# Kernel tuning notes

Hardware: AMD Instinct MI355X
Metric: run time of the kernel (lower is better)

## Reference

```python
import jax, jax.numpy as jnp
import numpy as np

N_EMBED = 8192
EMBED_DIM = 4
BETA = 0.25


def setup_inputs() -> dict:
    key = jax.random.key(0)
    k1, k2 = jax.random.split(key)
    z = jax.random.normal(k1, (8, EMBED_DIM, 64, 64), dtype=jnp.float32)
    # torch init: uniform(-1/n_embed, 1/n_embed)
    embed_w = jax.random.uniform(k2, (N_EMBED, EMBED_DIM), dtype=jnp.float32,
                                 minval=-1.0 / N_EMBED, maxval=1.0 / N_EMBED)
    return {"z": z, "embed_w": embed_w}


def reference(z, embed_w):
    # z: [B, C, H, W] -> [B, H, W, C]
    z_nhwc = jnp.transpose(z, (0, 2, 3, 1))
    z_flat = z_nhwc.reshape(-1, EMBED_DIM)  # [N, D]
    # squared L2 distances: ||z||^2 + ||e||^2 - 2 z e^T  -> [N, n_embed]
    d = (jnp.sum(z_flat * z_flat, axis=1, keepdims=True)
         + jnp.sum(embed_w * embed_w, axis=1)
         - 2.0 * z_flat @ embed_w.T)
    min_idx = jnp.argmin(d, axis=1)  # [N] int
    z_q = embed_w[min_idx].reshape(z_nhwc.shape)  # [B, H, W, C]
    sg = jax.lax.stop_gradient
    loss = (jnp.mean((sg(z_q) - z_nhwc) ** 2)
            + BETA * jnp.mean((z_q - sg(z_nhwc)) ** 2))
    # straight-through estimator
    z_q_ste = z_nhwc + sg(z_q - z_nhwc)
    z_q_out = jnp.transpose(z_q_ste, (0, 3, 1, 2))  # back to [B, C, H, W]
    return z_q_out, loss, min_idx
```

## Files before the change

### kernel.cpp

```cpp
#include <hip/hip_runtime.h>
#include <math.h>

typedef float v2f __attribute__((ext_vector_type(2)));

#define N_POINTS 32768
#define NUM_EMBED 8192
#define NPAIRS 4096
#define CH 64
#define CPC (NUM_EMBED / CH)
#define PAIRS (NPAIRS / CH)
#define PPT 8
#define RB 1024
#define RPB (RB / 64)
#define CSTRIDE 4096

__global__ void vq_prep_kernel(const float4* __restrict__ E, v2f* __restrict__ Epk) {
    int p = blockIdx.x * 256 + threadIdx.x;
    if (p < NPAIRS) {
        float4 a = E[2 * p];
        float4 b = E[2 * p + 1];
        Epk[4 * p + 0] = (v2f){a.x, b.x};
        Epk[4 * p + 1] = (v2f){a.y, b.y};
        Epk[4 * p + 2] = (v2f){a.z, b.z};
        Epk[4 * p + 3] = (v2f){a.w, b.w};
    }
}

__device__ __forceinline__ v2f pk_mul(v2f a, v2f b) {
    v2f d; asm("v_pk_mul_f32 %0, %1, %2" : "=v"(d) : "v"(a), "v"(b)); return d;
}
__device__ __forceinline__ v2f pk_fma(v2f a, v2f b, v2f c) {
    v2f d; asm("v_pk_fma_f32 %0, %1, %2, %3" : "=v"(d) : "v"(a), "v"(b), "v"(c)); return d;
}

__device__ __forceinline__ unsigned int fkey(float f) {
    unsigned int b = __float_as_uint(f);
    return b ^ (0x80000000u | (unsigned int)((int)b >> 31));
}

__global__ __launch_bounds__(256) void vq_filter_kernel(
        const float* __restrict__ z, const v2f* __restrict__ Epk,
        float* __restrict__ cmax) {
    __shared__ alignas(16) v2f sE[PAIRS * 4];

    const int c = blockIdx.y;
    if (threadIdx.x < PAIRS * 2) {
        ((float4*)sE)[threadIdx.x] =
            ((const float4*)(Epk + (size_t)c * PAIRS * 4))[threadIdx.x];
    }

    const int n0 = blockIdx.x * (256 * PPT) + threadIdx.x;

    v2f zv[PPT][4];
    #pragma unroll
    for (int p = 0; p < PPT; ++p) {
        int n = n0 + p * 256;
        int b = n >> 12, hw = n & 4095;
        const float* zp = z + b * 16384 + hw;
        zv[p][0] = (v2f){zp[0], zp[0]};
        zv[p][1] = (v2f){zp[CSTRIDE], zp[CSTRIDE]};
        zv[p][2] = (v2f){zp[2 * CSTRIDE], zp[2 * CSTRIDE]};
        zv[p][3] = (v2f){zp[3 * CSTRIDE], zp[3 * CSTRIDE]};
    }

    __syncthreads();

    float run[PPT];
    #pragma unroll
    for (int p = 0; p < PPT; ++p) run[p] = -__builtin_inff();

    const float4* sE4 = (const float4*)sE;
    #pragma unroll 2
    for (int t = 0; t < PAIRS; ++t) {
        float4 E01 = sE4[2 * t];
        float4 E23 = sE4[2 * t + 1];
        v2f e0 = {E01.x, E01.y};
        v2f e1 = {E01.z, E01.w};
        v2f e2 = {E23.x, E23.y};
        v2f e3 = {E23.z, E23.w};
        #pragma unroll
        for (int p = 0; p < PPT; ++p) {
            v2f dot = pk_mul(zv[p][0], e0);
            dot = pk_fma(zv[p][1], e1, dot);
            dot = pk_fma(zv[p][2], e2, dot);
            dot = pk_fma(zv[p][3], e3, dot);
            run[p] = fmaxf(fmaxf(dot.x, dot.y), run[p]);
        }
    }

    #pragma unroll
    for (int p = 0; p < PPT; ++p)
        cmax[(size_t)c * N_POINTS + n0 + p * 256] = run[p];
}

__global__ __launch_bounds__(RB) void vq_resolve_kernel(
        const float* __restrict__ z, const float4* __restrict__ E,
        const float* __restrict__ cmax,
        float* __restrict__ out, double* __restrict__ partial) {
    __shared__ float sCm[CH][RPB + 1];
    __shared__ double sdata[RPB];
    const int lane = threadIdx.x & 63;
    const int wid = threadIdx.x >> 6;
    const int n0 = blockIdx.x * RPB;
    const int n = n0 + wid;

    {
        int t = threadIdx.x;
        sCm[t >> 4][t & 15] = cmax[(size_t)(t >> 4) * N_POINTS + n0 + (t & 15)];
    }

    const int b = n >> 12;
    const int hw = n & 4095;
    const float* zp = z + b * 16384 + hw;
    float z0 = zp[0];
    float z1 = zp[CSTRIDE];
    float z2 = zp[2 * CSTRIDE];
    float z3 = zp[3 * CSTRIDE];
    float zz = __fmul_rn(z0, z0);
    zz = __fadd_rn(zz, __fmul_rn(z1, z1));
    zz = __fadd_rn(zz, __fmul_rn(z2, z2));
    zz = __fadd_rn(zz, __fmul_rn(z3, z3));

    __syncthreads();

    float cm = sCm[lane][wid];
    float gmax = cm;
    #pragma unroll
    for (int off = 32; off; off >>= 1)
        gmax = fmaxf(gmax, __shfl_xor(gmax, off));

    float u = __fmul_rn(__fadd_rn(zz, 0.01f), 2.38418579e-07f);
    float thr = __fsub_rn(gmax, __fadd_rn(__fadd_rn(u, u), 1e-7f));
    unsigned long long mask = __ballot(cm >= thr);

    unsigned long long bkey = ~0ull;
    while (mask) {
        int c = __builtin_ctzll(mask);
        mask &= mask - 1ull;
        int j0 = c * CPC + lane;
        #pragma unroll
        for (int h = 0; h < 2; ++h) {
            int j = j0 + h * 64;
            float4 e = E[j];
            float ee = __fmul_rn(e.x, e.x);
            ee = __fadd_rn(ee, __fmul_rn(e.y, e.y));
            ee = __fadd_rn(ee, __fmul_rn(e.z, e.z));
            ee = __fadd_rn(ee, __fmul_rn(e.w, e.w));
            float dot = __fmul_rn(z0, e.x);
            dot = __fmaf_rn(z1, e.y, dot);
            dot = __fmaf_rn(z2, e.z, dot);
            dot = __fmaf_rn(z3, e.w, dot);
            float d = __fmaf_rn(-2.0f, dot, __fadd_rn(zz, ee));
            unsigned long long key =
                ((unsigned long long)fkey(d) << 32) | (unsigned int)j;
            bkey = key < bkey ? key : bkey;
        }
    }
    #pragma unroll
    for (int off = 32; off; off >>= 1) {
        unsigned long long o = __shfl_xor(bkey, off);
        bkey = o < bkey ? o : bkey;
    }
    int besti = (int)(unsigned int)(bkey & 0xFFFFFFFFull);

    if (lane == 0) {
        float4 e = E[besti];
        float* op = out + b * 16384 + hw;
        float t0 = __fsub_rn(e.x, z0);
        float t1 = __fsub_rn(e.y, z1);
        float t2 = __fsub_rn(e.z, z2);
        float t3 = __fsub_rn(e.w, z3);
        op[0]           = __fadd_rn(z0, t0);
        op[CSTRIDE]     = __fadd_rn(z1, t1);
        op[2 * CSTRIDE] = __fadd_rn(z2, t2);
        op[3 * CSTRIDE] = __fadd_rn(z3, t3);
        out[131073 + n] = (float)besti;
        double ds = (double)__fmul_rn(t0, t0) + (double)__fmul_rn(t1, t1)
                  + (double)__fmul_rn(t2, t2) + (double)__fmul_rn(t3, t3);
        sdata[wid] = ds;
    }
    __syncthreads();
    if (threadIdx.x == 0) {
        double s = 0.0;
        #pragma unroll
        for (int w = 0; w < RPB; ++w) s += sdata[w];
        partial[blockIdx.x] = s;
    }
}

__global__ void vq_loss_kernel(const double* __restrict__ partial, float* __restrict__ out) {
    __shared__ double sdata[256];
    int t = threadIdx.x;
    double s = 0.0;
    for (int i = t; i < 2048; i += 256) s += partial[i];
    sdata[t] = s;
    __syncthreads();
    #pragma unroll
    for (int st = 128; st > 0; st >>= 1) {
        if (t < st) sdata[t] += sdata[t + st];
        __syncthreads();
    }
    if (t == 0) {
        float m = (float)(sdata[0] / 131072.0);
        out[131072] = __fadd_rn(m, __fmul_rn(0.25f, m));
    }
}

extern "C" void kernel_launch(void* const* d_in, const int* in_sizes, int n_in,
                              void* d_out, int out_size, void* d_ws, size_t ws_size,
                              hipStream_t stream) {
    const float* z = (const float*)d_in[0];
    const float4* E = (const float4*)d_in[1];
    float* out = (float*)d_out;

    char* ws = (char*)d_ws;
    v2f* Epk = (v2f*)ws;
    float* cmaxb = (float*)(ws + 131072);
    double* partial = (double*)(ws + 131072 + (size_t)CH * N_POINTS * 4);

    vq_prep_kernel<<<NPAIRS / 256, 256, 0, stream>>>(E, Epk);
    vq_filter_kernel<<<dim3(N_POINTS / (256 * PPT), CH), 256, 0, stream>>>(z, Epk, cmaxb);
    vq_resolve_kernel<<<N_POINTS / RPB, RB, 0, stream>>>(z, E, cmaxb, out, partial);
    vq_loss_kernel<<<1, 256, 0, stream>>>(partial, out);
}
```

Measured before the change: 53.06 us.

## Fold embedding prep into filter and loss reduction into resolve via last-block atomic

Removes the separate prep kernel by having each filter block load its own codebook chunk and transpose it into the packed pair layout in shared memory. Removes the standalone loss kernel by having each resolve block publish its partial sum and bump an atomic counter, so the last block to finish does the final reduction. This cuts two kernel launches and their inter-kernel gaps, at the cost of a memset launch, a strided shared-memory scatter in the filter prologue, and 8KB of extra shared memory in resolve.

```diff
diff --git a/kernel.cpp b/kernel.cpp
--- a/kernel.cpp
+++ b/kernel.cpp
@@ -5,26 +5,14 @@
 
 #define N_POINTS 32768
 #define NUM_EMBED 8192
-#define NPAIRS 4096
 #define CH 64
 #define CPC (NUM_EMBED / CH)
-#define PAIRS (NPAIRS / CH)
+#define PAIRS (CPC / 2)
 #define PPT 8
 #define RB 1024
 #define RPB (RB / 64)
+#define RGRID (N_POINTS / RPB)
 #define CSTRIDE 4096
-
-__global__ void vq_prep_kernel(const float4* __restrict__ E, v2f* __restrict__ Epk) {
-    int p = blockIdx.x * 256 + threadIdx.x;
-    if (p < NPAIRS) {
-        float4 a = E[2 * p];
-        float4 b = E[2 * p + 1];
-        Epk[4 * p + 0] = (v2f){a.x, b.x};
-        Epk[4 * p + 1] = (v2f){a.y, b.y};
-        Epk[4 * p + 2] = (v2f){a.z, b.z};
-        Epk[4 * p + 3] = (v2f){a.w, b.w};
-    }
-}
 
 __device__ __forceinline__ v2f pk_mul(v2f a, v2f b) {
     v2f d; asm("v_pk_mul_f32 %0, %1, %2" : "=v"(d) : "v"(a), "v"(b)); return d;
@@ -39,14 +27,19 @@
 }
 
 __global__ __launch_bounds__(256) void vq_filter_kernel(
-        const float* __restrict__ z, const v2f* __restrict__ Epk,
+        const float* __restrict__ z, const float4* __restrict__ E,
         float* __restrict__ cmax) {
     __shared__ alignas(16) v2f sE[PAIRS * 4];
 
     const int c = blockIdx.y;
-    if (threadIdx.x < PAIRS * 2) {
-        ((float4*)sE)[threadIdx.x] =
-            ((const float4*)(Epk + (size_t)c * PAIRS * 4))[threadIdx.x];
+    if (threadIdx.x < CPC) {
+        float4 e = E[c * CPC + threadIdx.x];
+        int p = threadIdx.x >> 1, h = threadIdx.x & 1;
+        float* sf = (float*)sE;
+        sf[8 * p + 0 + h] = e.x;
+        sf[8 * p + 2 + h] = e.y;
+        sf[8 * p + 4 + h] = e.z;
+        sf[8 * p + 6 + h] = e.w;
     }
 
     const int n0 = blockIdx.x * (256 * PPT) + threadIdx.x;
@@ -96,9 +89,12 @@
 __global__ __launch_bounds__(RB) void vq_resolve_kernel(
         const float* __restrict__ z, const float4* __restrict__ E,
         const float* __restrict__ cmax,
-        float* __restrict__ out, double* __restrict__ partial) {
+        float* __restrict__ out, double* __restrict__ partial,
+        unsigned int* __restrict__ done) {
     __shared__ float sCm[CH][RPB + 1];
     __shared__ double sdata[RPB];
+    __shared__ double sred[RB];
+    __shared__ int sLast;
     const int lane = threadIdx.x & 63;
     const int wid = threadIdx.x >> 6;
     const int n0 = blockIdx.x * RPB;
@@ -180,29 +176,34 @@
         sdata[wid] = ds;
     }
     __syncthreads();
+
     if (threadIdx.x == 0) {
         double s = 0.0;
         #pragma unroll
         for (int w = 0; w < RPB; ++w) s += sdata[w];
-        partial[blockIdx.x] = s;
-    }
-}
-
-__global__ void vq_loss_kernel(const double* __restrict__ partial, float* __restrict__ out) {
-    __shared__ double sdata[256];
-    int t = threadIdx.x;
-    double s = 0.0;
-    for (int i = t; i < 2048; i += 256) s += partial[i];
-    sdata[t] = s;
-    __syncthreads();
-    #pragma unroll
-    for (int st = 128; st > 0; st >>= 1) {
-        if (t < st) sdata[t] += sdata[t + st];
+        __hip_atomic_store(&partial[blockIdx.x], s, __ATOMIC_RELEASE,
+                           __HIP_MEMORY_SCOPE_AGENT);
+        unsigned int prev = __hip_atomic_fetch_add(done, 1u, __ATOMIC_ACQ_REL,
+                                                   __HIP_MEMORY_SCOPE_AGENT);
+        sLast = (prev == RGRID - 1);
+    }
+    __syncthreads();
+    if (sLast) {
+        double s = __hip_atomic_load(&partial[threadIdx.x], __ATOMIC_RELAXED,
+                                     __HIP_MEMORY_SCOPE_AGENT)
+                 + __hip_atomic_load(&partial[threadIdx.x + RB], __ATOMIC_RELAXED,
+                                     __HIP_MEMORY_SCOPE_AGENT);
+        sred[threadIdx.x] = s;
         __syncthreads();
-    }
-    if (t == 0) {
-        float m = (float)(sdata[0] / 131072.0);
-        out[131072] = __fadd_rn(m, __fmul_rn(0.25f, m));
+        #pragma unroll
+        for (int st = RB / 2; st > 0; st >>= 1) {
+            if (threadIdx.x < st) sred[threadIdx.x] += sred[threadIdx.x + st];
+            __syncthreads();
+        }
+        if (threadIdx.x == 0) {
+            float m = (float)(sred[0] / 131072.0);
+            out[131072] = __fadd_rn(m, __fmul_rn(0.25f, m));
+        }
     }
 }
 
@@ -214,12 +215,11 @@
     float* out = (float*)d_out;
 
     char* ws = (char*)d_ws;
-    v2f* Epk = (v2f*)ws;
-    float* cmaxb = (float*)(ws + 131072);
-    double* partial = (double*)(ws + 131072 + (size_t)CH * N_POINTS * 4);
-
-    vq_prep_kernel<<<NPAIRS / 256, 256, 0, stream>>>(E, Epk);
-    vq_filter_kernel<<<dim3(N_POINTS / (256 * PPT), CH), 256, 0, stream>>>(z, Epk, cmaxb);
-    vq_resolve_kernel<<<N_POINTS / RPB, RB, 0, stream>>>(z, E, cmaxb, out, partial);
-    vq_loss_kernel<<<1, 256, 0, stream>>>(partial, out);
-}
+    float* cmaxb = (float*)ws;
+    double* partial = (double*)(ws + (size_t)CH * N_POINTS * 4);
+    unsigned int* done = (unsigned int*)(ws + (size_t)CH * N_POINTS * 4 + RGRID * 8);
+
+    hipMemsetAsync(done, 0, 4, stream);
+    vq_filter_kernel<<<dim3(N_POINTS / (256 * PPT), CH), 256, 0, stream>>>(z, E, cmaxb);
+    vq_resolve_kernel<<<RGRID, RB, 0, stream>>>(z, E, cmaxb, out, partial, done);
+}
```

New measurement: 144.6 us. 2.72x slower.
